# Optimization experiments

Measured on AMD Instinct MI355X. Metric: run time of the kernel, lower is better.

## Reference

```python
import jax, jax.numpy as jnp
import numpy as np

B, S, D, H = 2, 2048, 1024, 16
DEPTH = D // H

def setup_inputs() -> dict:
    key = jax.random.key(0)
    ks = jax.random.split(key, 6)
    sc = 0.02
    return {
        "x": jax.random.normal(ks[0], (B, S, D), dtype=jnp.float32),
        "mask": jnp.ones((S, S), dtype=jnp.int32),
        "wq": jax.random.normal(ks[1], (D, D), dtype=jnp.float32) * sc,
        "bq": jnp.zeros((D,), dtype=jnp.float32),
        "wk": jax.random.normal(ks[2], (D, D), dtype=jnp.float32) * sc,
        "bk": jnp.zeros((D,), dtype=jnp.float32),
        "wv": jax.random.normal(ks[3], (D, D), dtype=jnp.float32) * sc,
        "bv": jnp.zeros((D,), dtype=jnp.float32),
        "wo": jax.random.normal(ks[4], (D, D), dtype=jnp.float32) * sc,
        "bo": jnp.zeros((D,), dtype=jnp.float32),
    }

def _split_heads(t):
    # [B,S,D] -> [B,H,S,depth]
    b, s, _ = t.shape
    return t.reshape(b, s, H, DEPTH).transpose(0, 2, 1, 3)

def reference(x, mask, wq, bq, wk, bk, wv, bv, wo, bo):
    q = _split_heads(x @ wq + bq)
    k = _split_heads(x @ wk + bk)
    v = _split_heads(x @ wv + bv)
    scale = 1.0 / jnp.sqrt(jnp.asarray(DEPTH, x.dtype))
    scores = jnp.einsum('bhqd,bhkd->bhqk', q, k) * scale
    # Faithful to original: band_part(ones,-1,0) is the LOWER triangle
    # (incl. diagonal), and it is ADDED times -1e9 -> lower triangle masked.
    s_len = mask.shape[0]
    tri = jnp.tril(jnp.ones((s_len, s_len), dtype=x.dtype))
    scores = scores + tri * (-1e9)
    attn = jax.nn.softmax(scores, axis=-1)  # dropout is identity at inference
    out = jnp.einsum('bhqk,bhkd->bhqd', attn, v)
    out = out.transpose(0, 2, 1, 3).reshape(x.shape[0], -1, D)
    return out @ wo + bo
```

## Files before the change

### kernel.cpp

```cpp
#include <hip/hip_runtime.h>
#include <hip/hip_bf16.h>


using bf16   = __bf16;
using bf16x4 = __attribute__((ext_vector_type(4))) __bf16;
using bf16x8 = __attribute__((ext_vector_type(8))) __bf16;
using f32x4  = __attribute__((ext_vector_type(4))) float;

__device__ __forceinline__ void load_lds16(const void* g, void* l) {
  __builtin_amdgcn_global_load_lds(
      (const __attribute__((address_space(1))) void*)g,
      (__attribute__((address_space(3))) void*)l, 16, 0, 0);
}

__global__ __launch_bounds__(256) void prep_kernel(
    const float* __restrict__ x, bf16* __restrict__ xb,
    const float* __restrict__ wq, const float* __restrict__ wk,
    const float* __restrict__ wv, const float* __restrict__ wo,
    bf16* __restrict__ wT) {
  const int t = threadIdx.x;
  int bid = blockIdx.x;
  if (bid < 4096) {
    const int i = (bid * 256 + t) * 4;
    const float4 v = *(const float4*)(x + i);
    bf16x4 o;
    o[0] = (bf16)v.x; o[1] = (bf16)v.y; o[2] = (bf16)v.z; o[3] = (bf16)v.w;
    *(bf16x4*)(xb + i) = o;
    return;
  }
  bid -= 4096;
  const int sel = bid >> 8;
  const float* w = (sel == 0) ? wq : (sel == 1) ? wk : (sel == 2) ? wv : wo;
  bf16* out = wT + (size_t)sel * 1048576;
  __shared__ float tile[64][65];
  const int n0 = (bid & 15) * 64;
  const int k0 = ((bid >> 4) & 15) * 64;
#pragma unroll
  for (int p = 0; p < 4; ++p) {
    const int row = p * 16 + (t >> 4);
    const int c4  = (t & 15) * 4;
    const float4 v = *(const float4*)&w[(size_t)(k0 + row) * 1024 + n0 + c4];
    tile[row][c4 + 0] = v.x; tile[row][c4 + 1] = v.y;
    tile[row][c4 + 2] = v.z; tile[row][c4 + 3] = v.w;
  }
  __syncthreads();
#pragma unroll
  for (int p = 0; p < 4; ++p) {
    const int rn = p * 16 + (t >> 4);
    const int c4 = (t & 15) * 4;
    bf16x4 o;
#pragma unroll
    for (int j = 0; j < 4; ++j) o[j] = (bf16)tile[c4 + j][rn];
    *(bf16x4*)&out[(size_t)(n0 + rn) * 1024 + k0 + c4] = o;
  }
}

template <int MODE>
__global__ __launch_bounds__(256, 2) void gemm_bt(
    const bf16* __restrict__ A, const bf16* __restrict__ Bt,
    const float* __restrict__ bias0, const float* __restrict__ bias1,
    const float* __restrict__ bias2, bf16* __restrict__ qf,
    bf16* __restrict__ kf, bf16* __restrict__ vt, float* __restrict__ fout,
    int Nblocks) {
  __shared__ __align__(16) char smem[32768];
  char* sA = smem;
  char* sB = smem + 16384;
  const int tid = threadIdx.x;
  const int lane = tid & 63;
  const int w = tid >> 6;
  const int wm = w >> 1, wn = w & 1;
  const int bid = blockIdx.x;
  const int m0 = (bid / Nblocks) * 128;
  const int n0 = (bid % Nblocks) * 128;

  const char* Ab = (const char*)A;
  const char* Bb = (const char*)Bt;
  size_t srcA[4], srcB[4];
#pragma unroll
  for (int it = 0; it < 4; ++it) {
    const int o = it * 4096 + tid * 16;
    const int r = o >> 7;
    const int cg = ((o >> 4) & 7) ^ (r & 7);
    srcA[it] = (size_t)(m0 + r) * 2048 + cg * 16;
    srcB[it] = (size_t)(n0 + r) * 2048 + cg * 16;
  }

  f32x4 acc[4][4] = {};

  for (int kt = 0; kt < 16; ++kt) {
    const size_t kb = (size_t)kt * 128;
#pragma unroll
    for (int it = 0; it < 4; ++it) {
      load_lds16(Ab + srcA[it] + kb, sA + it * 4096 + w * 1024);
      load_lds16(Bb + srcB[it] + kb, sB + it * 4096 + w * 1024);
    }
    asm volatile("s_waitcnt vmcnt(0)" ::: "memory");
    __syncthreads();
#pragma unroll
    for (int ks = 0; ks < 2; ++ks) {
      bf16x8 aF[4], bF[4];
      const int g = (lane >> 4) + 4 * ks;
#pragma unroll
      for (int i = 0; i < 4; ++i) {
        const int ra = wm * 64 + i * 16 + (lane & 15);
        aF[i] = *(const bf16x8*)(sA + ra * 128 + ((g ^ (ra & 7)) << 4));
        const int rb = wn * 64 + i * 16 + (lane & 15);
        bF[i] = *(const bf16x8*)(sB + rb * 128 + ((g ^ (rb & 7)) << 4));
      }
#pragma unroll
      for (int mi = 0; mi < 4; ++mi)
#pragma unroll
        for (int ni = 0; ni < 4; ++ni)
          acc[mi][ni] = __builtin_amdgcn_mfma_f32_16x16x32_bf16(
              aF[mi], bF[ni], acc[mi][ni], 0, 0, 0);
    }
    __syncthreads();
  }

  const int cn = lane & 15;
  const int gq = lane >> 4;
#pragma unroll
  for (int mi = 0; mi < 4; ++mi) {
#pragma unroll
    for (int ni = 0; ni < 4; ++ni) {
      const int n  = n0 + wn * 64 + ni * 16 + cn;
      const int mb = m0 + wm * 64 + mi * 16 + 4 * gq;
      const f32x4 v = acc[mi][ni];
      if (MODE == 0) {
        const float bias =
            (n < 1024) ? bias0[n] : ((n < 2048) ? bias1[n - 1024] : bias2[n - 2048]);
        if (n < 2048) {
          bf16* dst = (n < 1024) ? qf : kf;
          const int nn = n & 1023;
#pragma unroll
          for (int j = 0; j < 4; ++j)
            dst[(size_t)(mb + j) * 1024 + nn] = (bf16)(v[j] + bias);
        } else {
          const int nn = n - 2048;
          const int hh = nn >> 6, dd = nn & 63;
          const int bb = mb >> 11, ss = mb & 2047;
          bf16x4 pk;
#pragma unroll
          for (int j = 0; j < 4; ++j) pk[j] = (bf16)(v[j] + bias);
          *(bf16x4*)(vt + ((size_t)((bb * 16 + hh) * 64 + dd) * 2048 + ss)) = pk;
        }
      } else {
        const float bias = bias0[n];
#pragma unroll
        for (int j = 0; j < 4; ++j)
          fout[(size_t)(mb + j) * 1024 + n] = v[j] + bias;
      }
    }
  }
}

__global__ __launch_bounds__(256, 2) void attn_kernel(
    const bf16* __restrict__ qf, const bf16* __restrict__ kf,
    const bf16* __restrict__ vt, bf16* __restrict__ ao) {
  __shared__ __align__(16) char smem[41984];

  const int tid  = threadIdx.x;
  const int lane = tid & 63;
  const int hi   = lane >> 4;
  const int qlo  = lane & 15;
  const int w    = tid >> 6;
  const int pairIdx = blockIdx.x >> 5;
  const int bh = blockIdx.x & 31;
  const int b = bh >> 4, h = bh & 15;

  const char* kbase = (const char*)kf + ((size_t)b * 2048) * 2048 + h * 128;
  const char* vbase = (const char*)vt + (size_t)bh * 262144;
  const char* qbb   = (const char*)qf + ((size_t)b * 2048) * 2048 + h * 128;

  const int sr  = tid >> 3;
  const int scg = (tid & 7) ^ (sr & 7);

  char* sPw = smem + 32768 + w * 2304;

  bf16x8 onesB;
#pragma unroll
  for (int i = 0; i < 8; ++i) onesB[i] = (bf16)1.0f;

  for (int sp = 0; sp < 2; ++sp) {
    const int jq = sp ? (31 - pairIdx) : pairIdx;
    const int q0 = jq * 64;
    const int qb = q0 + w * 16;

    bf16x8 qA[2];
    {
      const char* qrow = qbb + (size_t)(qb + qlo) * 2048;
#pragma unroll
      for (int ks = 0; ks < 2; ++ks) {
        qA[ks] = *(const bf16x8*)(qrow + ks * 64 + hi * 16);
#pragma unroll
        for (int i = 0; i < 8; ++i)
          qA[ks][i] = (bf16)(0.125f * (float)qA[ks][i]);
      }
    }

    float m = -1e30f;
    f32x4 lacc = {};
    f32x4 O[4] = {};

    const int nt = (2048 - q0) >> 6;

    {
      char* dK = smem + w * 1024;
      char* dV = smem + 16384 + w * 1024;
#pragma unroll
      for (int p = 0; p < 2; ++p) {
        load_lds16(kbase + (size_t)(q0 + sr + 32 * p) * 2048 + scg * 16,
                   dK + p * 4096);
        load_lds16(vbase + (size_t)(sr + 32 * p) * 4096 + (size_t)q0 * 2 +
                       scg * 16,
                   dV + p * 4096);
      }
    }
    __syncthreads();

    for (int it = 0; it < nt; ++it) {
      const int cur = it & 1;

      if (it + 1 < nt) {
        const int kn = q0 + it * 64 + 64;
        char* dK = smem + (cur ^ 1) * 8192 + w * 1024;
        char* dV = smem + 16384 + (cur ^ 1) * 8192 + w * 1024;
#pragma unroll
        for (int p = 0; p < 2; ++p) {
          load_lds16(kbase + (size_t)(kn + sr + 32 * p) * 2048 + scg * 16,
                     dK + p * 4096);
          load_lds16(vbase + (size_t)(sr + 32 * p) * 4096 + (size_t)kn * 2 +
                         scg * 16,
                     dV + p * 4096);
        }
      }
      const char* bK = smem + cur * 8192;
      const char* bV = smem + 16384 + cur * 8192;

      f32x4 sc[4] = {};
#pragma unroll
      for (int ks = 0; ks < 2; ++ks) {
        const int g = hi + 4 * ks;
#pragma unroll
        for (int t = 0; t < 4; ++t) {
          const int rk = t * 16 + qlo;
          const bf16x8 kF =
              *(const bf16x8*)(bK + rk * 128 + ((g ^ (rk & 7)) << 4));
          sc[t] = __builtin_amdgcn_mfma_f32_16x16x32_bf16(kF, qA[ks], sc[t],
                                                          0, 0, 0);
        }
      }

      if (it == 0) {
#pragma unroll
        for (int t = 0; t < 4; ++t)
#pragma unroll
          for (int j = 0; j < 4; ++j) {
            const int kk = q0 + t * 16 + 4 * hi + j;
            const int qq = qb + qlo;
            if (kk <= qq) sc[t][j] = -1e30f;
          }
      }

      float tm = sc[0][0];
#pragma unroll
      for (int t = 0; t < 4; ++t)
#pragma unroll
        for (int j = 0; j < 4; ++j) tm = fmaxf(tm, sc[t][j]);
      tm = fmaxf(tm, __shfl_xor(tm, 16));
      tm = fmaxf(tm, __shfl_xor(tm, 32));

      if (!__all(tm - m <= 8.0f)) {
        const float mn = fmaxf(m, tm);
        const float al = __expf(m - mn);
        m = mn;
#pragma unroll
        for (int j = 0; j < 4; ++j) {
          const float alj = __shfl(al, 4 * hi + j);
          lacc[j] *= alj;
#pragma unroll
          for (int dt = 0; dt < 4; ++dt) O[dt][j] *= alj;
        }
      }

      bf16* pw = (bf16*)(sPw + qlo * 144);
#pragma unroll
      for (int t = 0; t < 4; ++t) {
        bf16x4 pk;
#pragma unroll
        for (int j = 0; j < 4; ++j) pk[j] = (bf16)__expf(sc[t][j] - m);
        *(bf16x4*)(pw + t * 16 + hi * 4) = pk;
      }

#pragma unroll
      for (int ks = 0; ks < 2; ++ks) {
        const bf16x8 pA =
            *(const bf16x8*)(sPw + qlo * 144 + hi * 16 + ks * 64);
        lacc = __builtin_amdgcn_mfma_f32_16x16x32_bf16(pA, onesB, lacc, 0, 0, 0);
        const int g = hi + 4 * ks;
#pragma unroll
        for (int dt = 0; dt < 4; ++dt) {
          const int rv = dt * 16 + qlo;
          const bf16x8 vF =
              *(const bf16x8*)(bV + rv * 128 + ((g ^ (rv & 7)) << 4));
          O[dt] = __builtin_amdgcn_mfma_f32_16x16x32_bf16(pA, vF, O[dt],
                                                          0, 0, 0);
        }
      }
      __syncthreads();
    }

#pragma unroll
    for (int j = 0; j < 4; ++j) {
      const float linv = (lacc[j] > 0.f) ? 1.f / lacc[j] : 0.f;
      const int qg = qb + 4 * hi + j;
#pragma unroll
      for (int dt = 0; dt < 4; ++dt)
        ao[(size_t)(b * 2048 + qg) * 1024 + h * 64 + dt * 16 + qlo] =
            (bf16)(O[dt][j] * linv);
    }
  }
}

__global__ __launch_bounds__(256) void vmean_kernel(const bf16* __restrict__ vt,
                                                    bf16* __restrict__ ao) {
  const int tid = threadIdx.x;
  const int lane = tid & 63, w = tid >> 6;
  const int gw = blockIdx.x * 4 + w;
  const int bh = gw >> 6, d = gw & 63;
  const int b = bh >> 4, h = bh & 15;
  const bf16x8* p = (const bf16x8*)(vt + (size_t)gw * 2048 + lane * 32);
  float s = 0.f;
#pragma unroll
  for (int i = 0; i < 4; ++i) {
    const bf16x8 v = p[i];
#pragma unroll
    for (int j = 0; j < 8; ++j) s += (float)v[j];
  }
  for (int off = 1; off < 64; off <<= 1) s += __shfl_xor(s, off);
  if (lane == 0)
    ao[(size_t)(b * 2048 + 2047) * 1024 + h * 64 + d] = (bf16)(s * (1.f / 2048.f));
}

extern "C" void kernel_launch(void* const* d_in, const int* in_sizes, int n_in,
                              void* d_out, int out_size, void* d_ws,
                              size_t ws_size, hipStream_t stream) {
  const float* x  = (const float*)d_in[0];
  const float* wq = (const float*)d_in[2];
  const float* bq = (const float*)d_in[3];
  const float* wk = (const float*)d_in[4];
  const float* bk = (const float*)d_in[5];
  const float* wv = (const float*)d_in[6];
  const float* bv = (const float*)d_in[7];
  const float* wo = (const float*)d_in[8];
  const float* bo = (const float*)d_in[9];
  float* out = (float*)d_out;

  if (ws_size < (size_t)25165824 * 2) return;

  bf16* ws    = (bf16*)d_ws;
  bf16* xb    = ws;
  bf16* wqkvT = xb + 4194304;
  bf16* woT   = wqkvT + 3145728;
  bf16* qfp   = woT + 1048576;
  bf16* kfp   = qfp + 4194304;
  bf16* vtp   = kfp + 4194304;
  bf16* aop   = vtp + 4194304;

  prep_kernel<<<5120, 256, 0, stream>>>(x, xb, wq, wk, wv, wo, wqkvT);

  gemm_bt<0><<<32 * 24, 256, 0, stream>>>(xb, wqkvT, bq, bk, bv, qfp, kfp, vtp,
                                          nullptr, 24);
  attn_kernel<<<512, 256, 0, stream>>>(qfp, kfp, vtp, aop);
  vmean_kernel<<<512, 256, 0, stream>>>(vtp, aop);
  gemm_bt<1><<<32 * 8, 256, 0, stream>>>(aop, woT, bo, nullptr, nullptr, nullptr,
                                         nullptr, nullptr, out, 8);
}
```

Before: 110.9 us.

## Double attention query tile per warp and keep P in registers via lane permutes

The attention kernel now has each wave process 32 query rows (two 16-row subtiles) against each K/V tile, so every K/V fragment read from shared memory feeds two MFMAs. The query block grows to 128 rows and the grid halves to 256 blocks. The softmax probabilities are no longer round-tripped through an LDS scratch buffer: they are packed to bf16 and rearranged into MFMA A-operand layout with permlane32/16 swaps (falling back to shuffles). The trade-off is higher register pressure, launch bounds lowered to one block per SM, and fewer blocks, which may underfill the GPU and unbalance the causal work.

```diff
diff --git a/kernel.cpp b/kernel.cpp
--- a/kernel.cpp
+++ b/kernel.cpp
@@ -3,14 +3,42 @@
 
 
 using bf16   = __bf16;
+using bf16x2 = __attribute__((ext_vector_type(2))) __bf16;
 using bf16x4 = __attribute__((ext_vector_type(4))) __bf16;
 using bf16x8 = __attribute__((ext_vector_type(8))) __bf16;
 using f32x4  = __attribute__((ext_vector_type(4))) float;
+using uintx2 = __attribute__((ext_vector_type(2))) unsigned int;
+using uintx4 = __attribute__((ext_vector_type(4))) unsigned int;
 
 __device__ __forceinline__ void load_lds16(const void* g, void* l) {
   __builtin_amdgcn_global_load_lds(
       (const __attribute__((address_space(1))) void*)g,
       (__attribute__((address_space(3))) void*)l, 16, 0, 0);
+}
+
+__device__ __forceinline__ unsigned int packbf(float a, float b) {
+  bf16x2 v;
+  v[0] = (bf16)a;
+  v[1] = (bf16)b;
+  return __builtin_bit_cast(unsigned int, v);
+}
+
+__device__ __forceinline__ void xchg_p(unsigned int u, unsigned int v, int hi,
+                                       unsigned int& f, unsigned int& s) {
+#if __has_builtin(__builtin_amdgcn_permlane32_swap) && \
+    __has_builtin(__builtin_amdgcn_permlane16_swap)
+  uintx2 ab = __builtin_amdgcn_permlane32_swap(u, v, false, false);
+  uintx2 fs = __builtin_amdgcn_permlane16_swap(ab[0], ab[1], false, false);
+  f = fs[0];
+  s = fs[1];
+#else
+  unsigned int a = (hi < 2) ? u : (unsigned int)__shfl_xor((int)v, 32);
+  unsigned int b = (hi < 2) ? (unsigned int)__shfl_xor((int)u, 32) : v;
+  unsigned int a16 = (unsigned int)__shfl_xor((int)a, 16);
+  unsigned int b16 = (unsigned int)__shfl_xor((int)b, 16);
+  f = (hi & 1) ? b16 : a;
+  s = (hi & 1) ? b : a16;
+#endif
 }
 
 __global__ __launch_bounds__(256) void prep_kernel(
@@ -154,10 +182,10 @@
   }
 }
 
-__global__ __launch_bounds__(256, 2) void attn_kernel(
+__global__ __launch_bounds__(256, 1) void attn_kernel(
     const bf16* __restrict__ qf, const bf16* __restrict__ kf,
     const bf16* __restrict__ vt, bf16* __restrict__ ao) {
-  __shared__ __align__(16) char smem[41984];
+  __shared__ __align__(16) char smem[32768];
 
   const int tid  = threadIdx.x;
   const int lane = tid & 63;
@@ -175,34 +203,33 @@
   const int sr  = tid >> 3;
   const int scg = (tid & 7) ^ (sr & 7);
 
-  char* sPw = smem + 32768 + w * 2304;
-
   bf16x8 onesB;
 #pragma unroll
   for (int i = 0; i < 8; ++i) onesB[i] = (bf16)1.0f;
 
   for (int sp = 0; sp < 2; ++sp) {
-    const int jq = sp ? (31 - pairIdx) : pairIdx;
-    const int q0 = jq * 64;
-    const int qb = q0 + w * 16;
-
-    bf16x8 qA[2];
-    {
-      const char* qrow = qbb + (size_t)(qb + qlo) * 2048;
+    const int jq = sp ? (15 - pairIdx) : pairIdx;
+    const int q0 = jq * 128;
+    const int qb = q0 + w * 32;
+
+    bf16x8 qA[2][2];
+#pragma unroll
+    for (int nt = 0; nt < 2; ++nt) {
+      const char* qrow = qbb + (size_t)(qb + 16 * nt + qlo) * 2048;
 #pragma unroll
       for (int ks = 0; ks < 2; ++ks) {
-        qA[ks] = *(const bf16x8*)(qrow + ks * 64 + hi * 16);
+        qA[nt][ks] = *(const bf16x8*)(qrow + ks * 64 + hi * 16);
 #pragma unroll
         for (int i = 0; i < 8; ++i)
-          qA[ks][i] = (bf16)(0.125f * (float)qA[ks][i]);
-      }
-    }
-
-    float m = -1e30f;
-    f32x4 lacc = {};
-    f32x4 O[4] = {};
-
-    const int nt = (2048 - q0) >> 6;
+          qA[nt][ks][i] = (bf16)(0.125f * (float)qA[nt][ks][i]);
+      }
+    }
+
+    float m[2] = {-1e30f, -1e30f};
+    f32x4 lacc[2] = {};
+    f32x4 O[2][4] = {};
+
+    const int nt_tiles = (2048 - q0) >> 6;
 
     {
       char* dK = smem + w * 1024;
@@ -218,10 +245,10 @@
     }
     __syncthreads();
 
-    for (int it = 0; it < nt; ++it) {
+    for (int it = 0; it < nt_tiles; ++it) {
       const int cur = it & 1;
 
-      if (it + 1 < nt) {
+      if (it + 1 < nt_tiles) {
         const int kn = q0 + it * 64 + 64;
         char* dK = smem + (cur ^ 1) * 8192 + w * 1024;
         char* dV = smem + 16384 + (cur ^ 1) * 8192 + w * 1024;
@@ -237,7 +264,7 @@
       const char* bK = smem + cur * 8192;
       const char* bV = smem + 16384 + cur * 8192;
 
-      f32x4 sc[4] = {};
+      f32x4 sc[2][4] = {};
 #pragma unroll
       for (int ks = 0; ks < 2; ++ks) {
         const int g = hi + 4 * ks;
@@ -246,79 +273,111 @@
           const int rk = t * 16 + qlo;
           const bf16x8 kF =
               *(const bf16x8*)(bK + rk * 128 + ((g ^ (rk & 7)) << 4));
-          sc[t] = __builtin_amdgcn_mfma_f32_16x16x32_bf16(kF, qA[ks], sc[t],
-                                                          0, 0, 0);
-        }
-      }
-
-      if (it == 0) {
+          sc[0][t] = __builtin_amdgcn_mfma_f32_16x16x32_bf16(kF, qA[0][ks],
+                                                             sc[0][t], 0, 0, 0);
+          sc[1][t] = __builtin_amdgcn_mfma_f32_16x16x32_bf16(kF, qA[1][ks],
+                                                             sc[1][t], 0, 0, 0);
+        }
+      }
+
+      if (it < 2) {
+        const int k0t = q0 + it * 64;
+#pragma unroll
+        for (int nt = 0; nt < 2; ++nt)
+#pragma unroll
+          for (int t = 0; t < 4; ++t)
+#pragma unroll
+            for (int j = 0; j < 4; ++j) {
+              const int kk = k0t + t * 16 + 4 * hi + j;
+              const int qq = qb + 16 * nt + qlo;
+              if (kk <= qq) sc[nt][t][j] = -1e30f;
+            }
+      }
+
+      float tm[2];
+#pragma unroll
+      for (int nt = 0; nt < 2; ++nt) {
+        float v = sc[nt][0][0];
 #pragma unroll
         for (int t = 0; t < 4; ++t)
 #pragma unroll
+          for (int j = 0; j < 4; ++j) v = fmaxf(v, sc[nt][t][j]);
+        v = fmaxf(v, __shfl_xor(v, 16));
+        v = fmaxf(v, __shfl_xor(v, 32));
+        tm[nt] = v;
+      }
+
+      const bool grew = (tm[0] - m[0] > 8.0f) || (tm[1] - m[1] > 8.0f);
+      if (__any(grew)) {
+#pragma unroll
+        for (int nt = 0; nt < 2; ++nt) {
+          const float mn = fmaxf(m[nt], tm[nt]);
+          const float al = __expf(m[nt] - mn);
+          m[nt] = mn;
+#pragma unroll
           for (int j = 0; j < 4; ++j) {
-            const int kk = q0 + t * 16 + 4 * hi + j;
-            const int qq = qb + qlo;
-            if (kk <= qq) sc[t][j] = -1e30f;
+            const float alj = __shfl(al, 4 * hi + j);
+            lacc[nt][j] *= alj;
+#pragma unroll
+            for (int dt = 0; dt < 4; ++dt) O[nt][dt][j] *= alj;
           }
-      }
-
-      float tm = sc[0][0];
-#pragma unroll
-      for (int t = 0; t < 4; ++t)
-#pragma unroll
-        for (int j = 0; j < 4; ++j) tm = fmaxf(tm, sc[t][j]);
-      tm = fmaxf(tm, __shfl_xor(tm, 16));
-      tm = fmaxf(tm, __shfl_xor(tm, 32));
-
-      if (!__all(tm - m <= 8.0f)) {
-        const float mn = fmaxf(m, tm);
-        const float al = __expf(m - mn);
-        m = mn;
-#pragma unroll
-        for (int j = 0; j < 4; ++j) {
-          const float alj = __shfl(al, 4 * hi + j);
-          lacc[j] *= alj;
-#pragma unroll
-          for (int dt = 0; dt < 4; ++dt) O[dt][j] *= alj;
-        }
-      }
-
-      bf16* pw = (bf16*)(sPw + qlo * 144);
-#pragma unroll
-      for (int t = 0; t < 4; ++t) {
-        bf16x4 pk;
-#pragma unroll
-        for (int j = 0; j < 4; ++j) pk[j] = (bf16)__expf(sc[t][j] - m);
-        *(bf16x4*)(pw + t * 16 + hi * 4) = pk;
+        }
+      }
+
+      bf16x8 pA[2][2];
+#pragma unroll
+      for (int nt = 0; nt < 2; ++nt) {
+        unsigned int W[4][2];
+#pragma unroll
+        for (int t = 0; t < 4; ++t)
+#pragma unroll
+          for (int p = 0; p < 2; ++p)
+            W[t][p] = packbf(__expf(sc[nt][t][2 * p] - m[nt]),
+                             __expf(sc[nt][t][2 * p + 1] - m[nt]));
+#pragma unroll
+        for (int ks = 0; ks < 2; ++ks) {
+          uintx4 w4;
+#pragma unroll
+          for (int p = 0; p < 2; ++p) {
+            unsigned int f, s;
+            xchg_p(W[2 * ks][p], W[2 * ks + 1][p], hi, f, s);
+            w4[p] = f;
+            w4[2 + p] = s;
+          }
+          pA[nt][ks] = __builtin_bit_cast(bf16x8, w4);
+          lacc[nt] = __builtin_amdgcn_mfma_f32_16x16x32_bf16(pA[nt][ks], onesB,
+                                                             lacc[nt], 0, 0, 0);
+        }
       }
 
 #pragma unroll
       for (int ks = 0; ks < 2; ++ks) {
-        const bf16x8 pA =
-            *(const bf16x8*)(sPw + qlo * 144 + hi * 16 + ks * 64);
-        lacc = __builtin_amdgcn_mfma_f32_16x16x32_bf16(pA, onesB, lacc, 0, 0, 0);
         const int g = hi + 4 * ks;
 #pragma unroll
         for (int dt = 0; dt < 4; ++dt) {
           const int rv = dt * 16 + qlo;
           const bf16x8 vF =
               *(const bf16x8*)(bV + rv * 128 + ((g ^ (rv & 7)) << 4));
-          O[dt] = __builtin_amdgcn_mfma_f32_16x16x32_bf16(pA, vF, O[dt],
-                                                          0, 0, 0);
+          O[0][dt] = __builtin_amdgcn_mfma_f32_16x16x32_bf16(pA[0][ks], vF,
+                                                             O[0][dt], 0, 0, 0);
+          O[1][dt] = __builtin_amdgcn_mfma_f32_16x16x32_bf16(pA[1][ks], vF,
+                                                             O[1][dt], 0, 0, 0);
         }
       }
       __syncthreads();
     }
 
 #pragma unroll
-    for (int j = 0; j < 4; ++j) {
-      const float linv = (lacc[j] > 0.f) ? 1.f / lacc[j] : 0.f;
-      const int qg = qb + 4 * hi + j;
-#pragma unroll
-      for (int dt = 0; dt < 4; ++dt)
-        ao[(size_t)(b * 2048 + qg) * 1024 + h * 64 + dt * 16 + qlo] =
-            (bf16)(O[dt][j] * linv);
-    }
+    for (int nt = 0; nt < 2; ++nt)
+#pragma unroll
+      for (int j = 0; j < 4; ++j) {
+        const float linv = (lacc[nt][j] > 0.f) ? 1.f / lacc[nt][j] : 0.f;
+        const int qg = qb + 16 * nt + 4 * hi + j;
+#pragma unroll
+        for (int dt = 0; dt < 4; ++dt)
+          ao[(size_t)(b * 2048 + qg) * 1024 + h * 64 + dt * 16 + qlo] =
+              (bf16)(O[nt][dt][j] * linv);
+      }
   }
 }
 
@@ -371,7 +430,7 @@
 
   gemm_bt<0><<<32 * 24, 256, 0, stream>>>(xb, wqkvT, bq, bk, bv, qfp, kfp, vtp,
                                           nullptr, 24);
-  attn_kernel<<<512, 256, 0, stream>>>(qfp, kfp, vtp, aop);
+  attn_kernel<<<256, 256, 0, stream>>>(qfp, kfp, vtp, aop);
   vmean_kernel<<<512, 256, 0, stream>>>(vtp, aop);
   gemm_bt<1><<<32 * 8, 256, 0, stream>>>(aop, woT, bo, nullptr, nullptr, nullptr,
                                          nullptr, nullptr, out, 8);
```

Result: slower. 120.4 us (+8.6%).
